# Optimization experiments

Measured on AMD Instinct MI355X. Metric: run time of the kernel, lower is better.

## Reference

```python
import jax, jax.numpy as jnp
import numpy as np

VOCAB = 100000
DIM = 128
B = 262144
NEG = 5

def setup_inputs() -> dict:
    key = jax.random.key(0)
    k1, k2, k3, k4 = jax.random.split(key, 4)
    bound = 0.5 / DIM
    input_emb = jax.random.uniform(k4, (VOCAB, DIM), jnp.float32, -bound, bound)
    # original inits output embeddings to zeros; use small random so scores are nontrivial
    output_emb = jax.random.normal(jax.random.fold_in(key, 7), (VOCAB, DIM), jnp.float32) * 0.01
    target_words = jax.random.randint(k1, (B,), 0, VOCAB)
    context_words = jax.random.randint(k2, (B,), 0, VOCAB)
    negative_words = jax.random.randint(k3, (B, NEG), 0, VOCAB)
    return {"target_words": target_words, "context_words": context_words,
            "negative_words": negative_words, "input_emb": input_emb,
            "output_emb": output_emb}

def reference(target_words, context_words, negative_words, input_emb, output_emb):
    t = input_emb[target_words]               # [B, D]
    c = output_emb[context_words]             # [B, D]
    pos_scores = jnp.einsum('bd,bd->b', t, c) # [B]
    positive_loss = -jnp.mean(jax.nn.log_sigmoid(pos_scores))
    n = output_emb[negative_words]            # [B, NEG, D]
    neg_scores = jnp.einsum('bd,bnd->bn', t, n)  # [B, NEG]
    negative_loss = -jnp.mean(jax.nn.log_sigmoid(-neg_scores))
    return (positive_loss, negative_loss)
```

## Files before the change

kernel.cpp:

```cpp
#include <hip/hip_runtime.h>

#define VOCAB 100000
#define DIM 128
#define BATCH 262144
#define NEG 5

__device__ __forceinline__ float softplus_stable(float x) {
    return log1pf(__expf(-fabsf(x))) + fmaxf(x, 0.0f);
}

__global__ void ns_init_kernel(float* acc) {
    acc[0] = 0.0f;
    acc[1] = 0.0f;
}

__global__ __launch_bounds__(256) void ns_loss_kernel(
    const int* __restrict__ tgt,
    const int* __restrict__ ctx,
    const int* __restrict__ negw,
    const float* __restrict__ iemb,
    const float* __restrict__ oemb,
    float* __restrict__ acc)
{
    const int tid = threadIdx.x;
    const int r = tid & 31;
    const int hw_in_block = tid >> 5;
    const int hw_global = blockIdx.x * 8 + hw_in_block;
    const int hw_total = gridDim.x * 8;

    float pos_acc = 0.0f, neg_acc = 0.0f;

    for (int e = hw_global; e < BATCH; e += hw_total) {
        const int tw = tgt[e];
        const int cw = ctx[e];

        const float4 t4 = *reinterpret_cast<const float4*>(iemb + (size_t)tw * DIM + r * 4);
        const float4 c4 = *reinterpret_cast<const float4*>(oemb + (size_t)cw * DIM + r * 4);

        float dp = t4.x * c4.x + t4.y * c4.y + t4.z * c4.z + t4.w * c4.w;

        float dn[NEG];
        #pragma unroll
        for (int j = 0; j < NEG; ++j) {
            const int nw = negw[e * NEG + j];
            const float4 n4 = *reinterpret_cast<const float4*>(oemb + (size_t)nw * DIM + r * 4);
            dn[j] = t4.x * n4.x + t4.y * n4.y + t4.z * n4.z + t4.w * n4.w;
        }

        #pragma unroll
        for (int m = 16; m >= 1; m >>= 1) {
            dp += __shfl_xor(dp, m, 64);
            #pragma unroll
            for (int j = 0; j < NEG; ++j) dn[j] += __shfl_xor(dn[j], m, 64);
        }

        if (r == 0) {
            pos_acc += softplus_stable(-dp);
            float s = 0.0f;
            #pragma unroll
            for (int j = 0; j < NEG; ++j) s += softplus_stable(dn[j]);
            neg_acc += s;
        }
    }

    __shared__ float sp[256];
    __shared__ float sn[256];
    sp[tid] = pos_acc;
    sn[tid] = neg_acc;
    __syncthreads();
    #pragma unroll
    for (int s = 128; s > 0; s >>= 1) {
        if (tid < s) {
            sp[tid] += sp[tid + s];
            sn[tid] += sn[tid + s];
        }
        __syncthreads();
    }
    if (tid == 0) {
        atomicAdd(&acc[0], sp[0]);
        atomicAdd(&acc[1], sn[0]);
    }
}

__global__ void ns_finalize_kernel(const float* __restrict__ acc, float* __restrict__ out) {
    out[0] = acc[0] * (1.0f / (float)BATCH);
    out[1] = acc[1] * (1.0f / ((float)BATCH * (float)NEG));
}

extern "C" void kernel_launch(void* const* d_in, const int* in_sizes, int n_in,
                              void* d_out, int out_size, void* d_ws, size_t ws_size,
                              hipStream_t stream) {
    const int*   tgt  = (const int*)d_in[0];
    const int*   ctx  = (const int*)d_in[1];
    const int*   negw = (const int*)d_in[2];
    const float* iemb = (const float*)d_in[3];
    const float* oemb = (const float*)d_in[4];
    float* out = (float*)d_out;
    float* acc = (float*)d_ws;

    ns_init_kernel<<<1, 1, 0, stream>>>(acc);
    ns_loss_kernel<<<2048, 256, 0, stream>>>(tgt, ctx, negw, iemb, oemb, acc);
    ns_finalize_kernel<<<1, 1, 0, stream>>>(acc, out);
}
```

Before: 166.3 us.

## Map each batch row to eight lanes with four float4 loads per lane

Each batch element is now handled by an 8-lane group instead of a 32-lane half-wave. Each lane issues four float4 loads per embedding row, so there are more independent loads in flight per thread and the shuffle reduction drops from five rounds to three. All 8 lanes compute the softplus redundantly to avoid a divergent branch, and the finalize step divides by an extra factor of 8 to compensate. Softplus now uses __logf(1+exp) instead of log1pf, which trades a little precision for cheaper transcendentals.

```diff
diff --git a/kernel.cpp b/kernel.cpp
--- a/kernel.cpp
+++ b/kernel.cpp
@@ -5,8 +5,12 @@
 #define BATCH 262144
 #define NEG 5
 
-__device__ __forceinline__ float softplus_stable(float x) {
-    return log1pf(__expf(-fabsf(x))) + fmaxf(x, 0.0f);
+__device__ __forceinline__ float softplus_fast(float x) {
+    return fmaxf(x, 0.0f) + __logf(1.0f + __expf(-fabsf(x)));
+}
+
+__device__ __forceinline__ float dot4(const float4 a, const float4 b) {
+    return a.x * b.x + a.y * b.y + a.z * b.z + a.w * b.w;
 }
 
 __global__ void ns_init_kernel(float* acc) {
@@ -23,44 +27,43 @@
     float* __restrict__ acc)
 {
     const int tid = threadIdx.x;
-    const int r = tid & 31;
-    const int hw_in_block = tid >> 5;
-    const int hw_global = blockIdx.x * 8 + hw_in_block;
-    const int hw_total = gridDim.x * 8;
+    const int r   = tid & 7;
+    const int grp = tid >> 3;
+    const int e0  = blockIdx.x * 32 + grp;
+    const int estride = gridDim.x * 32;
 
     float pos_acc = 0.0f, neg_acc = 0.0f;
 
-    for (int e = hw_global; e < BATCH; e += hw_total) {
+    for (int e = e0; e < BATCH; e += estride) {
         const int tw = tgt[e];
         const int cw = ctx[e];
 
-        const float4 t4 = *reinterpret_cast<const float4*>(iemb + (size_t)tw * DIM + r * 4);
-        const float4 c4 = *reinterpret_cast<const float4*>(oemb + (size_t)cw * DIM + r * 4);
+        const float4* tp = reinterpret_cast<const float4*>(iemb + (size_t)tw * DIM) + r * 4;
+        const float4 t0 = tp[0], t1 = tp[1], t2 = tp[2], t3 = tp[3];
 
-        float dp = t4.x * c4.x + t4.y * c4.y + t4.z * c4.z + t4.w * c4.w;
+        const float4* cp = reinterpret_cast<const float4*>(oemb + (size_t)cw * DIM) + r * 4;
+        float dp = dot4(t0, cp[0]) + dot4(t1, cp[1]) + dot4(t2, cp[2]) + dot4(t3, cp[3]);
 
         float dn[NEG];
         #pragma unroll
         for (int j = 0; j < NEG; ++j) {
             const int nw = negw[e * NEG + j];
-            const float4 n4 = *reinterpret_cast<const float4*>(oemb + (size_t)nw * DIM + r * 4);
-            dn[j] = t4.x * n4.x + t4.y * n4.y + t4.z * n4.z + t4.w * n4.w;
+            const float4* np_ = reinterpret_cast<const float4*>(oemb + (size_t)nw * DIM) + r * 4;
+            dn[j] = dot4(t0, np_[0]) + dot4(t1, np_[1]) + dot4(t2, np_[2]) + dot4(t3, np_[3]);
         }
 
         #pragma unroll
-        for (int m = 16; m >= 1; m >>= 1) {
+        for (int m = 4; m >= 1; m >>= 1) {
             dp += __shfl_xor(dp, m, 64);
             #pragma unroll
             for (int j = 0; j < NEG; ++j) dn[j] += __shfl_xor(dn[j], m, 64);
         }
 
-        if (r == 0) {
-            pos_acc += softplus_stable(-dp);
-            float s = 0.0f;
-            #pragma unroll
-            for (int j = 0; j < NEG; ++j) s += softplus_stable(dn[j]);
-            neg_acc += s;
-        }
+        pos_acc += softplus_fast(-dp);
+        float s = 0.0f;
+        #pragma unroll
+        for (int j = 0; j < NEG; ++j) s += softplus_fast(dn[j]);
+        neg_acc += s;
     }
 
     __shared__ float sp[256];
@@ -83,8 +86,8 @@
 }
 
 __global__ void ns_finalize_kernel(const float* __restrict__ acc, float* __restrict__ out) {
-    out[0] = acc[0] * (1.0f / (float)BATCH);
-    out[1] = acc[1] * (1.0f / ((float)BATCH * (float)NEG));
+    out[0] = acc[0] * (1.0f / ((float)BATCH * 8.0f));
+    out[1] = acc[1] * (1.0f / ((float)BATCH * (float)NEG * 8.0f));
 }
 
 extern "C" void kernel_launch(void* const* d_in, const int* in_sizes, int n_in,
```

Result: faster. 151.8 us (-8.8%).
